# Kernel tuning notes

Measured on AMD Instinct MI355X. Metric: run time of the kernel, lower is better.

Reference implementation:

```python
import jax, jax.numpy as jnp
import numpy as np

CH = 256          # channels
K = 3             # kernel_size
GROUP_CH = 16
G = CH // GROUP_CH   # groups = 16
RED = 2              # red_ratio
PAD = (K - 1) // 2
B, H, W = 8, 64, 64  # input must be spatially square (h==w) because the
                     # original forward does kernel @ x_unfolded over (h,w)


def setup_inputs() -> dict:
    key = jax.random.key(0)
    k1, k2, k3 = jax.random.split(key, 3)
    x = jax.random.normal(k1, (B, CH, H, W), dtype=jnp.float32)
    W_reduce = jax.random.normal(k2, (CH // RED, CH), dtype=jnp.float32) * 0.05
    b_reduce = jnp.zeros((CH // RED,), dtype=jnp.float32)
    W_span = jax.random.normal(k3, (K * K * G, CH // RED), dtype=jnp.float32) * 0.05
    b_span = jnp.zeros((K * K * G,), dtype=jnp.float32)
    return {"x": x, "W_reduce": W_reduce, "b_reduce": b_reduce,
            "W_span": W_span, "b_span": b_span}


def _unfold(x):
    """torch.nn.Unfold(K, dilation=1, padding=PAD, stride=1).
    Returns [b, c, K*K, h, w] with kernel positions in row-major order,
    channel-major overall (matches torch's C*K^2 flattening)."""
    b, c, h, w = x.shape
    xp = jnp.pad(x, ((0, 0), (0, 0), (PAD, PAD), (PAD, PAD)))
    patches = jnp.stack(
        [xp[:, :, ki:ki + h, kj:kj + w] for ki in range(K) for kj in range(K)],
        axis=2)
    return patches


def reference(x, W_reduce, b_reduce, W_span, b_span):
    b, c, h, w = x.shape
    # stride == 1 -> self.out is Identity
    red = jnp.einsum('bchw,oc->bohw', x, W_reduce) + b_reduce[None, :, None, None]
    ker = jnp.einsum('bohw,ko->bkhw', red, W_span) + b_span[None, :, None, None]
    # kernel: [b, G, K^2, h, w] (unsqueeze(2) -> broadcast over group_ch)
    ker = ker.reshape(b, G, K * K, h, w)
    # x_unfolded: [b, G, group_ch, K^2, h, w]
    xu = _unfold(x).reshape(b, G, GROUP_CH, K * K, h, w)
    # faithful to `(kernel @ x_unfolded).sum(dim=3)`: matmul over the last two
    # (spatial) dims, summed over kernel positions k
    out = jnp.einsum('bgkim,bgckmj->bgcij', ker, xu)
    return out.reshape(b, c, h, w)
```

## Files before the change

### kernel.cpp

```cpp
#include <hip/hip_runtime.h>

typedef unsigned short u16;
typedef unsigned int u32;
typedef __attribute__((ext_vector_type(8))) short bf16x8;
typedef __attribute__((ext_vector_type(4))) float f32x4;

#define CH   256
#define KKG  144
#define HW   4096
#define CSP  132

__device__ __forceinline__ u16 f2bf(float f) {
    u32 u = __float_as_uint(f);
    u += 0x7FFFu + ((u >> 16) & 1u);
    return (u16)(u >> 16);
}
__device__ __forceinline__ float bf2f(u16 u) {
    return __uint_as_float(((u32)u) << 16);
}

__global__ __launch_bounds__(256) void fuse_weights_k(
    const float* __restrict__ Wr, const float* __restrict__ br,
    const float* __restrict__ Ws, const float* __restrict__ bs,
    u16* __restrict__ Mfrag, float* __restrict__ biasF)
{
    __shared__ float ws[128];
    const int r = blockIdx.x;
    const int c = threadIdx.x;
    if (c < 128) ws[c] = Ws[r * 128 + c];
    __syncthreads();
    float acc = 0.f;
#pragma unroll 8
    for (int o = 0; o < 128; ++o) acc += ws[o] * Wr[o * CH + c];
    const int ks = c >> 5, quad = (c >> 3) & 3, jj = c & 7;
    const int mt = r >> 4, lane = (r & 15) + (quad << 4);
    Mfrag[((ks * 9 + mt) * 64 + lane) * 8 + jj] = f2bf(acc);
    if (c == 0) {
        float bb = bs[r];
        for (int o = 0; o < 128; ++o) bb += ws[o] * br[o];
        biasF[r] = bb;
    }
}

__global__ __launch_bounds__(256) void ker_abar_k(
    const float* __restrict__ x, const u16* __restrict__ Mfrag,
    const float* __restrict__ biasF, u16* __restrict__ Afrag)
{
    __shared__ u16 Cs[KKG * CSP];
    __shared__ float bias_s[KKG];
    const int b = blockIdx.x >> 5, jt = blockIdx.x & 31;
    const int col0 = jt * 128;
    const int t = threadIdx.x, lane = t & 63, w = t >> 6;
    const int nl = lane & 15, quad = lane >> 4;
    if (t < KKG) bias_s[t] = biasF[t];

    f32x4 acc[9][2];
#pragma unroll
    for (int mt = 0; mt < 9; ++mt)
#pragma unroll
        for (int nt = 0; nt < 2; ++nt) acc[mt][nt] = (f32x4)0.f;

    const int n0 = col0 + w * 32;
    for (int ks = 0; ks < 8; ++ks) {
        bf16x8 a[9];
        const bf16x8* Ag = ((const bf16x8*)Mfrag) + (ks * 9) * 64 + lane;
#pragma unroll
        for (int mt = 0; mt < 9; ++mt) a[mt] = Ag[mt * 64];
#pragma unroll
        for (int nt = 0; nt < 2; ++nt) {
            const float* xb = x + ((size_t)(b * CH + ks * 32 + quad * 8)) * HW + n0 + nt * 16 + nl;
            float f0 = xb[0],        f1 = xb[(size_t)HW],
                  f2 = xb[2*(size_t)HW], f3 = xb[3*(size_t)HW],
                  f4 = xb[4*(size_t)HW], f5 = xb[5*(size_t)HW],
                  f6 = xb[6*(size_t)HW], f7 = xb[7*(size_t)HW];
            union { bf16x8 v; uint4 u; } bb;
            bb.u.x = (u32)f2bf(f0) | ((u32)f2bf(f1) << 16);
            bb.u.y = (u32)f2bf(f2) | ((u32)f2bf(f3) << 16);
            bb.u.z = (u32)f2bf(f4) | ((u32)f2bf(f5) << 16);
            bb.u.w = (u32)f2bf(f6) | ((u32)f2bf(f7) << 16);
#pragma unroll
            for (int mt = 0; mt < 9; ++mt)
                acc[mt][nt] = __builtin_amdgcn_mfma_f32_16x16x32_bf16(a[mt], bb.v, acc[mt][nt], 0, 0, 0);
        }
    }
    __syncthreads();
#pragma unroll
    for (int mt = 0; mt < 9; ++mt)
#pragma unroll
        for (int nt = 0; nt < 2; ++nt) {
            const int colb = w * 32 + nt * 16 + nl;
            const int rb = mt * 16 + quad * 4;
#pragma unroll
            for (int reg = 0; reg < 4; ++reg)
                Cs[(rb + reg) * CSP + colb] = f2bf(acc[mt][nt][reg] + bias_s[rb + reg]);
        }
    __syncthreads();
    for (int v = t; v < 768; v += 256) {
        const int gd = v >> 4, rem = v & 15;
        const int il = rem >> 3, o = rem & 7;
        const int g = gd / 3, d = gd - g * 3;
        const int r0 = g * 9 + d;
        const int i = jt * 2 + il;
        const int base = il * 64 + o * 8;
        u16 h[8];
#pragma unroll
        for (int e = 0; e < 8; ++e) {
            const int m = o * 8 + e;
            float s = bf2f(Cs[(r0 + 3) * CSP + base + e]);
            if (m < 63) s += bf2f(Cs[r0 * CSP + base + e + 1]);
            if (m > 0)  s += bf2f(Cs[(r0 + 6) * CSP + base + e - 1]);
            h[e] = f2bf(s);
        }
        uint4 pk;
        pk.x = (u32)h[0] | ((u32)h[1] << 16);
        pk.y = (u32)h[2] | ((u32)h[3] << 16);
        pk.z = (u32)h[4] | ((u32)h[5] << 16);
        pk.w = (u32)h[6] | ((u32)h[7] << 16);
        const int ks2 = 2 * d + (o >> 2), quad2 = o & 3;
        const int mt2 = i >> 4, lane2 = (i & 15) + (quad2 << 4);
        const size_t idx = ((((size_t)(b * 16 + g) * 6 + ks2) * 4 + mt2) * 64 + lane2) * 8;
        *(uint4*)(Afrag + idx) = pk;
    }
}

__global__ __launch_bounds__(256) void inv_main_k(
    const float* __restrict__ x, const u16* __restrict__ Afrag,
    float* __restrict__ out)
{
    __shared__ u16 XT[4 * 4096];
    const int t = threadIdx.x;
    const int q = blockIdx.x & 3, bg = blockIdx.x >> 2;
    const int g = bg & 15, b = bg >> 4;
    const int ch_base = g * 16 + q * 4;

    for (int task = t; task < 512; task += 256) {
        const int ch = task >> 7, rem = task & 127;
        const int o = rem >> 4, jq = rem & 15;
        const float* xc = x + ((size_t)(b * CH + ch_base + ch)) * HW + o * 512 + jq * 4;
        float4 r0 = *(const float4*)(xc);
        float4 r1 = *(const float4*)(xc + 64);
        float4 r2 = *(const float4*)(xc + 128);
        float4 r3 = *(const float4*)(xc + 192);
        float4 r4 = *(const float4*)(xc + 256);
        float4 r5 = *(const float4*)(xc + 320);
        float4 r6 = *(const float4*)(xc + 384);
        float4 r7 = *(const float4*)(xc + 448);
        u16* base = XT + ch * 4096;
        uint4 pk;
        int j, chunk;
        pk.x = (u32)f2bf(r0.x) | ((u32)f2bf(r1.x) << 16);
        pk.y = (u32)f2bf(r2.x) | ((u32)f2bf(r3.x) << 16);
        pk.z = (u32)f2bf(r4.x) | ((u32)f2bf(r5.x) << 16);
        pk.w = (u32)f2bf(r6.x) | ((u32)f2bf(r7.x) << 16);
        j = jq * 4 + 0; chunk = j * 8 + (o ^ (j & 7));
        *(uint4*)(base + chunk * 8) = pk;
        pk.x = (u32)f2bf(r0.y) | ((u32)f2bf(r1.y) << 16);
        pk.y = (u32)f2bf(r2.y) | ((u32)f2bf(r3.y) << 16);
        pk.z = (u32)f2bf(r4.y) | ((u32)f2bf(r5.y) << 16);
        pk.w = (u32)f2bf(r6.y) | ((u32)f2bf(r7.y) << 16);
        j = jq * 4 + 1; chunk = j * 8 + (o ^ (j & 7));
        *(uint4*)(base + chunk * 8) = pk;
        pk.x = (u32)f2bf(r0.z) | ((u32)f2bf(r1.z) << 16);
        pk.y = (u32)f2bf(r2.z) | ((u32)f2bf(r3.z) << 16);
        pk.z = (u32)f2bf(r4.z) | ((u32)f2bf(r5.z) << 16);
        pk.w = (u32)f2bf(r6.z) | ((u32)f2bf(r7.z) << 16);
        j = jq * 4 + 2; chunk = j * 8 + (o ^ (j & 7));
        *(uint4*)(base + chunk * 8) = pk;
        pk.x = (u32)f2bf(r0.w) | ((u32)f2bf(r1.w) << 16);
        pk.y = (u32)f2bf(r2.w) | ((u32)f2bf(r3.w) << 16);
        pk.z = (u32)f2bf(r4.w) | ((u32)f2bf(r5.w) << 16);
        pk.w = (u32)f2bf(r6.w) | ((u32)f2bf(r7.w) << 16);
        j = jq * 4 + 3; chunk = j * 8 + (o ^ (j & 7));
        *(uint4*)(base + chunk * 8) = pk;
    }
    __syncthreads();

    const int lane = t & 63, w = t >> 6;
    const int nl = lane & 15, quad = lane >> 4;
    f32x4 acc[4][4];
#pragma unroll
    for (int mt = 0; mt < 4; ++mt)
#pragma unroll
        for (int nt = 0; nt < 4; ++nt) acc[mt][nt] = (f32x4)0.f;

    const u16* XTc = XT + w * 4096;
    for (int ks = 0; ks < 6; ++ks) {
        const int d = ks >> 1, mh = ks & 1;
        const bf16x8* Ag = ((const bf16x8*)Afrag) + ((size_t)(bg * 6 + ks) * 4) * 64 + lane;
        bf16x8 a0 = Ag[0], a1 = Ag[64], a2 = Ag[128], a3 = Ag[192];
        const int o = mh * 4 + quad;
#pragma unroll
        for (int nt = 0; nt < 4; ++nt) {
            const int jrow = nt * 16 + nl + d - 1;
            const int jc = jrow < 0 ? 0 : (jrow > 63 ? 63 : jrow);
            const int chunk = jc * 8 + (o ^ (jc & 7));
            bf16x8 bv = *(const bf16x8*)(XTc + chunk * 8);
            if (jrow < 0 || jrow > 63) bv = (bf16x8)(short)0;
            acc[0][nt] = __builtin_amdgcn_mfma_f32_16x16x32_bf16(a0, bv, acc[0][nt], 0, 0, 0);
            acc[1][nt] = __builtin_amdgcn_mfma_f32_16x16x32_bf16(a1, bv, acc[1][nt], 0, 0, 0);
            acc[2][nt] = __builtin_amdgcn_mfma_f32_16x16x32_bf16(a2, bv, acc[2][nt], 0, 0, 0);
            acc[3][nt] = __builtin_amdgcn_mfma_f32_16x16x32_bf16(a3, bv, acc[3][nt], 0, 0, 0);
        }
    }
    float* op = out + ((size_t)(b * CH + ch_base + w)) * HW;
#pragma unroll
    for (int mt = 0; mt < 4; ++mt)
#pragma unroll
        for (int nt = 0; nt < 4; ++nt)
#pragma unroll
            for (int reg = 0; reg < 4; ++reg)
                op[(mt * 16 + quad * 4 + reg) * 64 + nt * 16 + nl] = acc[mt][nt][reg];
}

extern "C" void kernel_launch(void* const* d_in, const int* in_sizes, int n_in,
                              void* d_out, int out_size, void* d_ws, size_t ws_size,
                              hipStream_t stream)
{
    const float* x  = (const float*)d_in[0];
    const float* Wr = (const float*)d_in[1];
    const float* br = (const float*)d_in[2];
    const float* Ws = (const float*)d_in[3];
    const float* bs = (const float*)d_in[4];
    float* out = (float*)d_out;

    char* ws = (char*)d_ws;
    u16*   Mfrag = (u16*)(ws);
    float* biasF = (float*)(ws + 73728);
    u16*   Afrag = (u16*)(ws + 81920);

    fuse_weights_k<<<dim3(KKG), dim3(256), 0, stream>>>(Wr, br, Ws, bs, Mfrag, biasF);
    ker_abar_k<<<dim3(256), dim3(256), 0, stream>>>(x, Mfrag, biasF, Afrag);
    inv_main_k<<<dim3(512), dim3(256), 0, stream>>>(x, Afrag, out);
}
```

Measured before the change: 111.6 us.

## Split work finer across blocks and waves in kernel-gen and main kernels

The kernel-generation kernel now handles one spatial row (64 columns) per block instead of two, so the grid doubles to 512 blocks and each wave keeps fewer accumulators. The main involution kernel moves to 512 threads, with two waves per channel each covering half the output columns. This halves per-thread accumulators and loads per thread, aiming at better occupancy and latency hiding on the MI355X's many CUs. The cost is that A fragments and x loads are re-read by more waves, and each block has less work to amortise its setup.

```diff
diff --git a/kernel.cpp b/kernel.cpp
--- a/kernel.cpp
+++ b/kernel.cpp
@@ -8,7 +8,7 @@
 #define CH   256
 #define KKG  144
 #define HW   4096
-#define CSP  132
+#define CSP  68
 
 __device__ __forceinline__ u16 f2bf(float f) {
     u32 u = __float_as_uint(f);
@@ -42,73 +42,59 @@
     }
 }
 
-__global__ __launch_bounds__(256) void ker_abar_k(
+__global__ __launch_bounds__(256, 4) void ker_abar_k(
     const float* __restrict__ x, const u16* __restrict__ Mfrag,
     const float* __restrict__ biasF, u16* __restrict__ Afrag)
 {
     __shared__ u16 Cs[KKG * CSP];
     __shared__ float bias_s[KKG];
-    const int b = blockIdx.x >> 5, jt = blockIdx.x & 31;
-    const int col0 = jt * 128;
+    const int b = blockIdx.x >> 6, irow = blockIdx.x & 63;
     const int t = threadIdx.x, lane = t & 63, w = t >> 6;
     const int nl = lane & 15, quad = lane >> 4;
     if (t < KKG) bias_s[t] = biasF[t];
 
-    f32x4 acc[9][2];
-#pragma unroll
-    for (int mt = 0; mt < 9; ++mt)
-#pragma unroll
-        for (int nt = 0; nt < 2; ++nt) acc[mt][nt] = (f32x4)0.f;
-
-    const int n0 = col0 + w * 32;
+    f32x4 acc[9];
+#pragma unroll
+    for (int mt = 0; mt < 9; ++mt) acc[mt] = (f32x4)0.f;
+
+    const int ncol = irow * 64 + w * 16 + nl;
+#pragma unroll
     for (int ks = 0; ks < 8; ++ks) {
-        bf16x8 a[9];
+        const float* xb = x + ((size_t)(b * CH + ks * 32 + quad * 8)) * HW + ncol;
+        float f0 = xb[0],              f1 = xb[(size_t)HW],
+              f2 = xb[2 * (size_t)HW], f3 = xb[3 * (size_t)HW],
+              f4 = xb[4 * (size_t)HW], f5 = xb[5 * (size_t)HW],
+              f6 = xb[6 * (size_t)HW], f7 = xb[7 * (size_t)HW];
+        union { bf16x8 v; uint4 u; } bb;
+        bb.u.x = (u32)f2bf(f0) | ((u32)f2bf(f1) << 16);
+        bb.u.y = (u32)f2bf(f2) | ((u32)f2bf(f3) << 16);
+        bb.u.z = (u32)f2bf(f4) | ((u32)f2bf(f5) << 16);
+        bb.u.w = (u32)f2bf(f6) | ((u32)f2bf(f7) << 16);
         const bf16x8* Ag = ((const bf16x8*)Mfrag) + (ks * 9) * 64 + lane;
 #pragma unroll
-        for (int mt = 0; mt < 9; ++mt) a[mt] = Ag[mt * 64];
-#pragma unroll
-        for (int nt = 0; nt < 2; ++nt) {
-            const float* xb = x + ((size_t)(b * CH + ks * 32 + quad * 8)) * HW + n0 + nt * 16 + nl;
-            float f0 = xb[0],        f1 = xb[(size_t)HW],
-                  f2 = xb[2*(size_t)HW], f3 = xb[3*(size_t)HW],
-                  f4 = xb[4*(size_t)HW], f5 = xb[5*(size_t)HW],
-                  f6 = xb[6*(size_t)HW], f7 = xb[7*(size_t)HW];
-            union { bf16x8 v; uint4 u; } bb;
-            bb.u.x = (u32)f2bf(f0) | ((u32)f2bf(f1) << 16);
-            bb.u.y = (u32)f2bf(f2) | ((u32)f2bf(f3) << 16);
-            bb.u.z = (u32)f2bf(f4) | ((u32)f2bf(f5) << 16);
-            bb.u.w = (u32)f2bf(f6) | ((u32)f2bf(f7) << 16);
-#pragma unroll
-            for (int mt = 0; mt < 9; ++mt)
-                acc[mt][nt] = __builtin_amdgcn_mfma_f32_16x16x32_bf16(a[mt], bb.v, acc[mt][nt], 0, 0, 0);
-        }
-    }
-    __syncthreads();
-#pragma unroll
-    for (int mt = 0; mt < 9; ++mt)
-#pragma unroll
-        for (int nt = 0; nt < 2; ++nt) {
-            const int colb = w * 32 + nt * 16 + nl;
-            const int rb = mt * 16 + quad * 4;
-#pragma unroll
-            for (int reg = 0; reg < 4; ++reg)
-                Cs[(rb + reg) * CSP + colb] = f2bf(acc[mt][nt][reg] + bias_s[rb + reg]);
-        }
-    __syncthreads();
-    for (int v = t; v < 768; v += 256) {
-        const int gd = v >> 4, rem = v & 15;
-        const int il = rem >> 3, o = rem & 7;
+        for (int mt = 0; mt < 9; ++mt)
+            acc[mt] = __builtin_amdgcn_mfma_f32_16x16x32_bf16(Ag[mt * 64], bb.v, acc[mt], 0, 0, 0);
+    }
+    __syncthreads();
+#pragma unroll
+    for (int mt = 0; mt < 9; ++mt) {
+        const int rb = mt * 16 + quad * 4;
+#pragma unroll
+        for (int reg = 0; reg < 4; ++reg)
+            Cs[(rb + reg) * CSP + w * 16 + nl] = f2bf(acc[mt][reg] + bias_s[rb + reg]);
+    }
+    __syncthreads();
+    for (int v = t; v < 384; v += 256) {
+        const int gd = v >> 3, o = v & 7;
         const int g = gd / 3, d = gd - g * 3;
         const int r0 = g * 9 + d;
-        const int i = jt * 2 + il;
-        const int base = il * 64 + o * 8;
         u16 h[8];
 #pragma unroll
         for (int e = 0; e < 8; ++e) {
             const int m = o * 8 + e;
-            float s = bf2f(Cs[(r0 + 3) * CSP + base + e]);
-            if (m < 63) s += bf2f(Cs[r0 * CSP + base + e + 1]);
-            if (m > 0)  s += bf2f(Cs[(r0 + 6) * CSP + base + e - 1]);
+            float s = bf2f(Cs[(r0 + 3) * CSP + m]);
+            if (m < 63) s += bf2f(Cs[r0 * CSP + m + 1]);
+            if (m > 0)  s += bf2f(Cs[(r0 + 6) * CSP + m - 1]);
             h[e] = f2bf(s);
         }
         uint4 pk;
@@ -117,13 +103,13 @@
         pk.z = (u32)h[4] | ((u32)h[5] << 16);
         pk.w = (u32)h[6] | ((u32)h[7] << 16);
         const int ks2 = 2 * d + (o >> 2), quad2 = o & 3;
-        const int mt2 = i >> 4, lane2 = (i & 15) + (quad2 << 4);
+        const int mt2 = irow >> 4, lane2 = (irow & 15) + (quad2 << 4);
         const size_t idx = ((((size_t)(b * 16 + g) * 6 + ks2) * 4 + mt2) * 64 + lane2) * 8;
         *(uint4*)(Afrag + idx) = pk;
     }
 }
 
-__global__ __launch_bounds__(256) void inv_main_k(
+__global__ __launch_bounds__(512) void inv_main_k(
     const float* __restrict__ x, const u16* __restrict__ Afrag,
     float* __restrict__ out)
 {
@@ -132,11 +118,13 @@
     const int q = blockIdx.x & 3, bg = blockIdx.x >> 2;
     const int g = bg & 15, b = bg >> 4;
     const int ch_base = g * 16 + q * 4;
-
-    for (int task = t; task < 512; task += 256) {
-        const int ch = task >> 7, rem = task & 127;
-        const int o = rem >> 4, jq = rem & 15;
-        const float* xc = x + ((size_t)(b * CH + ch_base + ch)) * HW + o * 512 + jq * 4;
+    const int lane = t & 63, w = t >> 6;
+    const int cl = w >> 1, nth = w & 1;
+
+    {
+        const int tt = nth * 64 + lane;
+        const int o = tt >> 4, jq = tt & 15;
+        const float* xc = x + ((size_t)(b * CH + ch_base + cl)) * HW + o * 512 + jq * 4;
         float4 r0 = *(const float4*)(xc);
         float4 r1 = *(const float4*)(xc + 64);
         float4 r2 = *(const float4*)(xc + 128);
@@ -145,7 +133,7 @@
         float4 r5 = *(const float4*)(xc + 320);
         float4 r6 = *(const float4*)(xc + 384);
         float4 r7 = *(const float4*)(xc + 448);
-        u16* base = XT + ch * 4096;
+        u16* base = XT + cl * 4096;
         uint4 pk;
         int j, chunk;
         pk.x = (u32)f2bf(r0.x) | ((u32)f2bf(r1.x) << 16);
@@ -175,41 +163,42 @@
     }
     __syncthreads();
 
-    const int lane = t & 63, w = t >> 6;
     const int nl = lane & 15, quad = lane >> 4;
-    f32x4 acc[4][4];
+    f32x4 acc[4][2];
 #pragma unroll
     for (int mt = 0; mt < 4; ++mt)
 #pragma unroll
-        for (int nt = 0; nt < 4; ++nt) acc[mt][nt] = (f32x4)0.f;
-
-    const u16* XTc = XT + w * 4096;
+        for (int ntl = 0; ntl < 2; ++ntl) acc[mt][ntl] = (f32x4)0.f;
+
+    const u16* XTc = XT + cl * 4096;
+#pragma unroll
     for (int ks = 0; ks < 6; ++ks) {
         const int d = ks >> 1, mh = ks & 1;
         const bf16x8* Ag = ((const bf16x8*)Afrag) + ((size_t)(bg * 6 + ks) * 4) * 64 + lane;
         bf16x8 a0 = Ag[0], a1 = Ag[64], a2 = Ag[128], a3 = Ag[192];
         const int o = mh * 4 + quad;
 #pragma unroll
-        for (int nt = 0; nt < 4; ++nt) {
+        for (int ntl = 0; ntl < 2; ++ntl) {
+            const int nt = nth * 2 + ntl;
             const int jrow = nt * 16 + nl + d - 1;
             const int jc = jrow < 0 ? 0 : (jrow > 63 ? 63 : jrow);
             const int chunk = jc * 8 + (o ^ (jc & 7));
             bf16x8 bv = *(const bf16x8*)(XTc + chunk * 8);
             if (jrow < 0 || jrow > 63) bv = (bf16x8)(short)0;
-            acc[0][nt] = __builtin_amdgcn_mfma_f32_16x16x32_bf16(a0, bv, acc[0][nt], 0, 0, 0);
-            acc[1][nt] = __builtin_amdgcn_mfma_f32_16x16x32_bf16(a1, bv, acc[1][nt], 0, 0, 0);
-            acc[2][nt] = __builtin_amdgcn_mfma_f32_16x16x32_bf16(a2, bv, acc[2][nt], 0, 0, 0);
-            acc[3][nt] = __builtin_amdgcn_mfma_f32_16x16x32_bf16(a3, bv, acc[3][nt], 0, 0, 0);
+            acc[0][ntl] = __builtin_amdgcn_mfma_f32_16x16x32_bf16(a0, bv, acc[0][ntl], 0, 0, 0);
+            acc[1][ntl] = __builtin_amdgcn_mfma_f32_16x16x32_bf16(a1, bv, acc[1][ntl], 0, 0, 0);
+            acc[2][ntl] = __builtin_amdgcn_mfma_f32_16x16x32_bf16(a2, bv, acc[2][ntl], 0, 0, 0);
+            acc[3][ntl] = __builtin_amdgcn_mfma_f32_16x16x32_bf16(a3, bv, acc[3][ntl], 0, 0, 0);
         }
     }
-    float* op = out + ((size_t)(b * CH + ch_base + w)) * HW;
+    float* op = out + ((size_t)(b * CH + ch_base + cl)) * HW;
 #pragma unroll
     for (int mt = 0; mt < 4; ++mt)
 #pragma unroll
-        for (int nt = 0; nt < 4; ++nt)
+        for (int ntl = 0; ntl < 2; ++ntl)
 #pragma unroll
             for (int reg = 0; reg < 4; ++reg)
-                op[(mt * 16 + quad * 4 + reg) * 64 + nt * 16 + nl] = acc[mt][nt][reg];
+                op[(mt * 16 + quad * 4 + reg) * 64 + (nth * 2 + ntl) * 16 + nl] = acc[mt][ntl][reg];
 }
 
 extern "C" void kernel_launch(void* const* d_in, const int* in_sizes, int n_in,
@@ -229,6 +218,6 @@
     u16*   Afrag = (u16*)(ws + 81920);
 
     fuse_weights_k<<<dim3(KKG), dim3(256), 0, stream>>>(Wr, br, Ws, bs, Mfrag, biasF);
-    ker_abar_k<<<dim3(256), dim3(256), 0, stream>>>(x, Mfrag, biasF, Afrag);
-    inv_main_k<<<dim3(512), dim3(256), 0, stream>>>(x, Afrag, out);
-}
+    ker_abar_k<<<dim3(512), dim3(256), 0, stream>>>(x, Mfrag, biasF, Afrag);
+    inv_main_k<<<dim3(512), dim3(512), 0, stream>>>(x, Afrag, out);
+}
```

After: 115.3 us. 1.03x slower.
